# Kernel optimization log

Hardware: AMD Instinct MI355X
Metric: run time of the kernel (lower is better)

Reference implementation:

```python
import jax, jax.numpy as jnp
import numpy as np

IMAGE_SIZE = 512


def _build_masks(image_size):
    # Vectorized equivalent of the module's triple-loop pyramid construction.
    w = h = image_size
    x = w - 1  # pyramid is (w-1, h-1)
    idx = np.arange(x)
    J, K = np.meshgrid(idx, idx, indexing='ij')
    # ring index i at (j,k) is min distance to any border of the (x,x) square
    ring = np.minimum(np.minimum(J, K), np.minimum(x - 1 - J, x - 1 - K))
    pyramid = x // 2 - ring
    plane = np.full((w, h), w // 2, dtype=np.int64)
    plane[1:, 1:] = pyramid
    L = image_size // 2 + 1  # number of bins
    # one-hot rectangular-ring masks: mask[r] = (plane == r)
    mask = (plane[None, :, :] == np.arange(L)[:, None, None]).astype(np.float32)
    mask_n = np.maximum(mask.sum(axis=(1, 2)), 1e-8).astype(np.float32)
    return jnp.asarray(mask), jnp.asarray(mask_n)


def setup_inputs() -> dict:
    key = jax.random.key(0)
    x = jax.random.uniform(key, (16, 3, IMAGE_SIZE, IMAGE_SIZE), dtype=jnp.float32)
    mask, mask_n = _build_masks(IMAGE_SIZE)
    return {"x": x, "mask": mask, "mask_n": mask_n}


def reference(x, mask, mask_n):
    # only_psd=True branch: RGB -> luma, scaled by 20
    mag = 20.0 * (0.299 * x[:, 0] + 0.587 * x[:, 1] + 0.114 * x[:, 2])  # [B,H,W]
    # per-bin masked average; einsum avoids materializing [B,L,H,W]
    profile = jnp.einsum('bhw,lhw->bl', mag, mask) / mask_n  # [B,L]
    pmin = profile.min()
    pmax = profile.max()
    return (profile - pmin) / (pmax - pmin)
```

## Files before the change

kernel.cpp:

```cpp
#include <hip/hip_runtime.h>

#define IMG 512
#define HW (IMG * IMG)
#define NB 257
#define BATCH 16
#define RG 32


__global__ __launch_bounds__(256) void hist_kernel(const float* __restrict__ x,
                                                   float* __restrict__ partial) {
    const int gx   = blockIdx.x;
    const int b    = blockIdx.y;
    const int wid  = threadIdx.x >> 6;
    const int lane = threadIdx.x & 63;

    __shared__ float bins[NB];
    for (int i = threadIdx.x; i < NB; i += 256) bins[i] = 0.f;
    __syncthreads();

    const float* xbase = x + (size_t)b * 3 * HW;
    const int h0 = (gx << 4) + (wid << 2);

#pragma unroll
    for (int rr = 0; rr < 4; ++rr) {
        const int h = h0 + rr;
        const float* xr  = xbase + (size_t)h * IMG;
        const float* xg  = xr + HW;
        const float* xbl = xg + HW;
        const int m = min(h - 1, 511 - h);
        float mid = 0.f;
#pragma unroll
        for (int j = 0; j < 2; ++j) {
            const int w0 = (((j << 6) + lane) << 2);
            const float4 r  = *reinterpret_cast<const float4*>(xr  + w0);
            const float4 g  = *reinterpret_cast<const float4*>(xg  + w0);
            const float4 bv = *reinterpret_cast<const float4*>(xbl + w0);
            float mg[4];
            mg[0] = 20.f * (0.299f * r.x + 0.587f * g.x + 0.114f * bv.x);
            mg[1] = 20.f * (0.299f * r.y + 0.587f * g.y + 0.114f * bv.y);
            mg[2] = 20.f * (0.299f * r.z + 0.587f * g.z + 0.114f * bv.z);
            mg[3] = 20.f * (0.299f * r.w + 0.587f * g.w + 0.114f * bv.w);

            if (h == 0) {
                mid += mg[0] + mg[1] + mg[2] + mg[3];
            } else {
#pragma unroll
                for (int t = 0; t < 4; ++t) {
                    const int w = w0 + t;
                    if (w == 0) {
                        atomicAdd(&bins[256], mg[t]);
                    } else {
                        const int d = min(w - 1, 511 - w);
                        if (d >= m) mid += mg[t];
                        else        atomicAdd(&bins[255 - d], mg[t]);
                    }
                }
            }
        }
#pragma unroll
        for (int off = 32; off > 0; off >>= 1) mid += __shfl_down(mid, off, 64);
        if (lane == 0) atomicAdd(&bins[(h == 0) ? 256 : (255 - m)], mid);
    }
    __syncthreads();

    float* pp = partial + ((size_t)b * RG + gx) * NB;
    for (int i = threadIdx.x; i < NB; i += 256) pp[i] = bins[i];
}

__global__ __launch_bounds__(1024) void finalize_kernel(const float* __restrict__ partial,
                                                        const float* __restrict__ mask_n,
                                                        float* __restrict__ out) {
    __shared__ float prof_s[BATCH * NB];
    __shared__ float red_min[16];
    __shared__ float red_max[16];

    const int lane = threadIdx.x & 63;
    const int wv   = threadIdx.x >> 6;

    float lmin = 3.402823466e+38f, lmax = -3.402823466e+38f;
    for (int i = threadIdx.x; i < BATCH * NB; i += 1024) {
        const int bb = i / NB;
        const int l  = i - bb * NB;
        const float* p = partial + (size_t)bb * RG * NB + l;
        float s = 0.f;
#pragma unroll
        for (int g = 0; g < RG; ++g) s += p[(size_t)g * NB];
        s /= mask_n[l];
        prof_s[i] = s;
        lmin = fminf(lmin, s);
        lmax = fmaxf(lmax, s);
    }
#pragma unroll
    for (int off = 32; off > 0; off >>= 1) {
        lmin = fminf(lmin, __shfl_xor(lmin, off, 64));
        lmax = fmaxf(lmax, __shfl_xor(lmax, off, 64));
    }
    if (lane == 0) { red_min[wv] = lmin; red_max[wv] = lmax; }
    __syncthreads();

    float pmin = red_min[0], pmax = red_max[0];
#pragma unroll
    for (int k = 1; k < 16; ++k) {
        pmin = fminf(pmin, red_min[k]);
        pmax = fmaxf(pmax, red_max[k]);
    }
    const float inv = 1.f / (pmax - pmin);
    for (int i = threadIdx.x; i < BATCH * NB; i += 1024)
        out[i] = (prof_s[i] - pmin) * inv;
}

extern "C" void kernel_launch(void* const* d_in, const int* in_sizes, int n_in,
                              void* d_out, int out_size, void* d_ws, size_t ws_size,
                              hipStream_t stream) {
    const float* x      = (const float*)d_in[0];
    const float* mask_n = (const float*)d_in[2];
    float* out     = (float*)d_out;
    float* partial = (float*)d_ws;

    hist_kernel<<<dim3(RG, BATCH), 256, 0, stream>>>(x, partial);
    finalize_kernel<<<1, 1024, 0, stream>>>(partial, mask_n, out);
}
```

Before: 38.75 us.

## Give each wave one row and split finalize into parallel reduce plus norm

The histogram kernel now assigns one image row per wavefront instead of four, so the grid grows from 32 to 128 blocks per batch image and all loads are issued up front. The old single-block finalize is split into a per-batch reduce kernel, which sums the partial histograms across 16 blocks, and a small normalization kernel. The aim is more parallelism in both stages and a shorter serial tail. In exchange, the partial buffer holding partial histograms is four times larger, there is one extra kernel launch, and each block does the same shared-memory init and writeback while processing a quarter of the rows.

```diff
diff --git a/kernel.cpp b/kernel.cpp
--- a/kernel.cpp
+++ b/kernel.cpp
@@ -4,11 +4,11 @@
 #define HW (IMG * IMG)
 #define NB 257
 #define BATCH 16
-#define RG 32
+#define RG 128
 
 
-__global__ __launch_bounds__(256) void hist_kernel(const float* __restrict__ x,
-                                                   float* __restrict__ partial) {
+__global__ __launch_bounds__(256, 8) void hist_kernel(const float* __restrict__ x,
+                                                      float* __restrict__ partial) {
     const int gx   = blockIdx.x;
     const int b    = blockIdx.y;
     const int wid  = threadIdx.x >> 6;
@@ -18,77 +18,95 @@
     for (int i = threadIdx.x; i < NB; i += 256) bins[i] = 0.f;
     __syncthreads();
 
-    const float* xbase = x + (size_t)b * 3 * HW;
-    const int h0 = (gx << 4) + (wid << 2);
+    const int h = (gx << 2) + wid;
+    const float* xr  = x + (size_t)b * 3 * HW + (size_t)h * IMG;
+    const float* xg  = xr + HW;
+    const float* xbl = xg + HW;
 
+    const int wA = (lane << 2);
+    const int wB = wA + 256;
+
+    const float4 rA = *reinterpret_cast<const float4*>(xr  + wA);
+    const float4 gA = *reinterpret_cast<const float4*>(xg  + wA);
+    const float4 bA = *reinterpret_cast<const float4*>(xbl + wA);
+    const float4 rB = *reinterpret_cast<const float4*>(xr  + wB);
+    const float4 gB = *reinterpret_cast<const float4*>(xg  + wB);
+    const float4 bB = *reinterpret_cast<const float4*>(xbl + wB);
+
+    float mgA[4], mgB[4];
+    mgA[0] = 20.f * (0.299f * rA.x + 0.587f * gA.x + 0.114f * bA.x);
+    mgA[1] = 20.f * (0.299f * rA.y + 0.587f * gA.y + 0.114f * bA.y);
+    mgA[2] = 20.f * (0.299f * rA.z + 0.587f * gA.z + 0.114f * bA.z);
+    mgA[3] = 20.f * (0.299f * rA.w + 0.587f * gA.w + 0.114f * bA.w);
+    mgB[0] = 20.f * (0.299f * rB.x + 0.587f * gB.x + 0.114f * bB.x);
+    mgB[1] = 20.f * (0.299f * rB.y + 0.587f * gB.y + 0.114f * bB.y);
+    mgB[2] = 20.f * (0.299f * rB.z + 0.587f * gB.z + 0.114f * bB.z);
+    mgB[3] = 20.f * (0.299f * rB.w + 0.587f * gB.w + 0.114f * bB.w);
+
+    const int m = min(h - 1, 511 - h);
+    float mid = 0.f;
+
+    if (h == 0) {
+        mid = mgA[0] + mgA[1] + mgA[2] + mgA[3] +
+              mgB[0] + mgB[1] + mgB[2] + mgB[3];
+    } else {
 #pragma unroll
-    for (int rr = 0; rr < 4; ++rr) {
-        const int h = h0 + rr;
-        const float* xr  = xbase + (size_t)h * IMG;
-        const float* xg  = xr + HW;
-        const float* xbl = xg + HW;
-        const int m = min(h - 1, 511 - h);
-        float mid = 0.f;
-#pragma unroll
-        for (int j = 0; j < 2; ++j) {
-            const int w0 = (((j << 6) + lane) << 2);
-            const float4 r  = *reinterpret_cast<const float4*>(xr  + w0);
-            const float4 g  = *reinterpret_cast<const float4*>(xg  + w0);
-            const float4 bv = *reinterpret_cast<const float4*>(xbl + w0);
-            float mg[4];
-            mg[0] = 20.f * (0.299f * r.x + 0.587f * g.x + 0.114f * bv.x);
-            mg[1] = 20.f * (0.299f * r.y + 0.587f * g.y + 0.114f * bv.y);
-            mg[2] = 20.f * (0.299f * r.z + 0.587f * g.z + 0.114f * bv.z);
-            mg[3] = 20.f * (0.299f * r.w + 0.587f * g.w + 0.114f * bv.w);
-
-            if (h == 0) {
-                mid += mg[0] + mg[1] + mg[2] + mg[3];
+        for (int t = 0; t < 4; ++t) {
+            const int w = wA + t;
+            if (w == 0) {
+                atomicAdd(&bins[256], mgA[t]);
             } else {
-#pragma unroll
-                for (int t = 0; t < 4; ++t) {
-                    const int w = w0 + t;
-                    if (w == 0) {
-                        atomicAdd(&bins[256], mg[t]);
-                    } else {
-                        const int d = min(w - 1, 511 - w);
-                        if (d >= m) mid += mg[t];
-                        else        atomicAdd(&bins[255 - d], mg[t]);
-                    }
-                }
+                const int d = min(w - 1, 511 - w);
+                if (d >= m) mid += mgA[t];
+                else        atomicAdd(&bins[255 - d], mgA[t]);
             }
         }
 #pragma unroll
-        for (int off = 32; off > 0; off >>= 1) mid += __shfl_down(mid, off, 64);
-        if (lane == 0) atomicAdd(&bins[(h == 0) ? 256 : (255 - m)], mid);
+        for (int t = 0; t < 4; ++t) {
+            const int w = wB + t;
+            const int d = min(w - 1, 511 - w);
+            if (d >= m) mid += mgB[t];
+            else        atomicAdd(&bins[255 - d], mgB[t]);
+        }
     }
+
+#pragma unroll
+    for (int off = 32; off > 0; off >>= 1) mid += __shfl_down(mid, off, 64);
+    if (lane == 0) atomicAdd(&bins[(h == 0) ? 256 : (255 - m)], mid);
     __syncthreads();
 
     float* pp = partial + ((size_t)b * RG + gx) * NB;
     for (int i = threadIdx.x; i < NB; i += 256) pp[i] = bins[i];
 }
 
-__global__ __launch_bounds__(1024) void finalize_kernel(const float* __restrict__ partial,
-                                                        const float* __restrict__ mask_n,
-                                                        float* __restrict__ out) {
-    __shared__ float prof_s[BATCH * NB];
+__global__ __launch_bounds__(256) void reduce_kernel(const float* __restrict__ partial,
+                                                     const float* __restrict__ mask_n,
+                                                     float* __restrict__ profile) {
+    const int b = blockIdx.x;
+    const float* p0 = partial + (size_t)b * RG * NB;
+    for (int l = threadIdx.x; l < NB; l += 256) {
+        float s = 0.f;
+#pragma unroll 8
+        for (int g = 0; g < RG; ++g) s += p0[(size_t)g * NB + l];
+        profile[b * NB + l] = s / mask_n[l];
+    }
+}
+
+__global__ __launch_bounds__(1024) void norm_kernel(const float* __restrict__ profile,
+                                                    float* __restrict__ out) {
     __shared__ float red_min[16];
     __shared__ float red_max[16];
-
     const int lane = threadIdx.x & 63;
     const int wv   = threadIdx.x >> 6;
 
     float lmin = 3.402823466e+38f, lmax = -3.402823466e+38f;
-    for (int i = threadIdx.x; i < BATCH * NB; i += 1024) {
-        const int bb = i / NB;
-        const int l  = i - bb * NB;
-        const float* p = partial + (size_t)bb * RG * NB + l;
-        float s = 0.f;
+    float v[5];
 #pragma unroll
-        for (int g = 0; g < RG; ++g) s += p[(size_t)g * NB];
-        s /= mask_n[l];
-        prof_s[i] = s;
-        lmin = fminf(lmin, s);
-        lmax = fmaxf(lmax, s);
+    for (int k = 0; k < 5; ++k) {
+        const int i = threadIdx.x + (k << 10);
+        v[k] = (i < BATCH * NB) ? profile[i] : profile[0];
+        lmin = fminf(lmin, v[k]);
+        lmax = fmaxf(lmax, v[k]);
     }
 #pragma unroll
     for (int off = 32; off > 0; off >>= 1) {
@@ -105,8 +123,11 @@
         pmax = fmaxf(pmax, red_max[k]);
     }
     const float inv = 1.f / (pmax - pmin);
-    for (int i = threadIdx.x; i < BATCH * NB; i += 1024)
-        out[i] = (prof_s[i] - pmin) * inv;
+#pragma unroll
+    for (int k = 0; k < 5; ++k) {
+        const int i = threadIdx.x + (k << 10);
+        if (i < BATCH * NB) out[i] = (v[k] - pmin) * inv;
+    }
 }
 
 extern "C" void kernel_launch(void* const* d_in, const int* in_sizes, int n_in,
@@ -116,7 +137,9 @@
     const float* mask_n = (const float*)d_in[2];
     float* out     = (float*)d_out;
     float* partial = (float*)d_ws;
+    float* profile = partial + (size_t)BATCH * RG * NB;
 
     hist_kernel<<<dim3(RG, BATCH), 256, 0, stream>>>(x, partial);
-    finalize_kernel<<<1, 1024, 0, stream>>>(partial, mask_n, out);
+    reduce_kernel<<<BATCH, 256, 0, stream>>>(partial, mask_n, profile);
+    norm_kernel<<<1, 1024, 0, stream>>>(profile, out);
 }
```

New measurement: 41.99 us. +8.4%, slower.
